# Kernel optimization log

Measured on AMD Instinct MI355X. Metric: run time of the kernel, lower is better.

The kernel has to match this reference:

```python
import jax, jax.numpy as jnp
import numpy as np

MARGIN = 0.5
BETA, GAMMA = 0.5, 0.2   # hard-coded in _get_triplet_selection_function
NUM_ANCHORS = 30          # hard-coded in select()
EPS_COS = 1e-8

B, C, D = 320, 80, 128


def setup_inputs() -> dict:
    key = jax.random.key(0)
    k1, k2, k3 = jax.random.split(key, 3)
    label = jax.random.randint(k1, (B, C), 0, 2).astype(jnp.int32)
    source = jax.random.normal(k2, (B, D), dtype=jnp.float32)
    target = jax.random.normal(k3, (B, D), dtype=jnp.float32)
    return {"label": label, "source": source, "target": target}


def _cos_distance(src, tgt):
    # F.cosine_similarity(src.unsqueeze(1), tgt, dim=-1): [B, B] sim matrix
    ns = jnp.linalg.norm(src, axis=-1)          # [B]
    nt = jnp.linalg.norm(tgt, axis=-1)          # [B]
    sim = (src @ tgt.T) / jnp.maximum(ns[:, None] * nt[None, :], EPS_COS)
    return jnp.clip(1.0 - sim, 0.0)


def _label_distances(labels_f):
    dot = labels_f @ labels_f.T                 # [B, B]
    sn = jnp.sqrt(jnp.diagonal(dot))            # [B]
    norms = sn[None, :] * sn[:, None]
    return 1.0 - jnp.minimum(1.0, dot / norms)


def _base_mask(b):
    ine = ~jnp.eye(b, dtype=bool)               # indices_not_equal
    # (a!=p) & (a!=n) & (p!=n)  ->  [B, B, B]
    return ine[:, :, None] & ine[:, None, :] & ine[None, :, :]


def _anchor_mask(fd, num_anchors):
    # select_diverse_anchors: pick the num_anchors anchors with the largest
    # mean feature distance to all other samples (most "diverse").
    diversity = jnp.mean(fd, axis=1)            # [B]
    _, idx = jax.lax.top_k(diversity, num_anchors)
    m = jnp.zeros((fd.shape[0],), dtype=bool).at[idx].set(True)
    return m[:, None, None]                     # broadcastable over (a, p, n)


def _triplet_mask(ld, beta, gamma):
    # select_triplets_smartly: (a, p) must be label-similar (dist <= gamma)
    # and (a, n) must be label-dissimilar (dist >= beta).
    pos = ld <= gamma                           # [B, B] over (a, p)
    neg = ld >= beta                            # [B, B] over (a, n)
    return pos[:, :, None] & neg[:, None, :]


def reference(label, source, target):
    fd = _cos_distance(source, target)                       # [B, B]
    ld = _label_distances(label.astype(jnp.float32))         # [B, B]
    mask = (_base_mask(fd.shape[0])
            & _anchor_mask(fd, NUM_ANCHORS)
            & _triplet_mask(ld, BETA, GAMMA))                # [B, B, B]
    # triplet_loss[a,p,n] = fd[a,p] - fd[a,n] + margin
    tl = fd[:, :, None] - fd[:, None, :] + MARGIN
    tl = jnp.clip(jnp.where(mask, tl, 0.0), 0.0)
    num_pos = jnp.sum(mask.astype(jnp.float32))
    return jnp.sum(tl) / (num_pos + 1e-4)
```

## Files before the change

kernel.cpp:

```cpp
#include <hip/hip_runtime.h>
#include <cstdint>

namespace {

constexpr int NB = 320;
constexpr int ND = 128;
constexpr int NC = 80;
constexpr int NANCH = 30;
constexpr int NW = 5;

constexpr size_t OFF_DIV  = 0;
constexpr size_t OFF_ASUM = 1280;
constexpr size_t OFF_ACNT = 3840;
constexpr size_t OFF_PACK = 5120;
constexpr size_t OFF_TGTT = 10240;

__global__ __launch_bounds__(256) void k_prep(
    const float* __restrict__ tgt,
    const int* __restrict__ label,
    float4* __restrict__ tgtT4,
    unsigned long long* __restrict__ packed)
{
    const int tid = threadIdx.x;
    const int w = tid >> 6, lane = tid & 63;
    const int r0 = blockIdx.x * 8;

    __shared__ float4 tile4[8][33];

    {
        const int r = r0 + w;
        int l0 = label[r * NC + lane];
        int l1 = (lane < NC - 64) ? label[r * NC + 64 + lane] : 0;
        unsigned long long b0 = __ballot(l0 != 0);
        unsigned long long b1 = __ballot(l1 != 0);
        if (lane == 0) { packed[2 * r] = b0; packed[2 * r + 1] = b1; }

        const int r2 = r0 + 4 + w;
        l0 = label[r2 * NC + lane];
        l1 = (lane < NC - 64) ? label[r2 * NC + 64 + lane] : 0;
        b0 = __ballot(l0 != 0);
        b1 = __ballot(l1 != 0);
        if (lane == 0) { packed[2 * r2] = b0; packed[2 * r2 + 1] = b1; }
    }

    {
        const int r = tid >> 5, d4 = tid & 31;
        tile4[r][d4] = reinterpret_cast<const float4*>(tgt)[(r0 + r) * 32 + d4];
    }
    __syncthreads();
    {
        const int rr = tid & 7, d4 = tid >> 3;
        tgtT4[d4 * NB + r0 + rr] = tile4[rr][d4];
    }
}

__global__ __launch_bounds__(256) void k_main(
    const float* __restrict__ src,
    const float4* __restrict__ tgtT4,
    const unsigned long long* __restrict__ packed,
    float* __restrict__ divr,
    double* __restrict__ asum,
    int* __restrict__ acnt)
{
    const int a = blockIdx.x;
    const int tid = threadIdx.x;
    const int w = tid >> 6, lane = tid & 63;

    __shared__ float sa[ND];
    __shared__ float snsa;
    __shared__ float red[256];
    __shared__ unsigned long long pk[2 * NB];
    __shared__ float fdrow[NB];
    __shared__ unsigned long long pmask[NW], nmask[NW];
    __shared__ double wsum[4];

    if (tid < ND) sa[tid] = src[a * ND + tid];
    if (w == 0) {
        float s0 = src[a * ND + lane];
        float s1 = src[a * ND + lane + 64];
        float v = s0 * s0 + s1 * s1;
        for (int off = 32; off > 0; off >>= 1) v += __shfl_down(v, off);
        if (lane == 0) snsa = sqrtf(v);
    }
    for (int q = tid; q < 2 * NB; q += 256) pk[q] = packed[q];
    __syncthreads();

    const unsigned long long a0 = pk[2 * a], a1 = pk[2 * a + 1];
    const float nsa = snsa;

    float acc = 0.f;
#pragma unroll
    for (int it = 0; it < 2; ++it) {
        const int j = tid + 256 * it;
        if (j < NB) {
            float dot = 0.f, tn = 0.f;
#pragma unroll
            for (int d = 0; d < ND / 4; ++d) {
                float4 t = tgtT4[d * NB + j];
                dot += sa[4 * d + 0] * t.x + sa[4 * d + 1] * t.y +
                       sa[4 * d + 2] * t.z + sa[4 * d + 3] * t.w;
                tn += t.x * t.x + t.y * t.y + t.z * t.z + t.w * t.w;
            }
            float sim = dot / fmaxf(nsa * sqrtf(tn), 1e-8f);
            float f = fmaxf(1.0f - sim, 0.0f);
            fdrow[j] = f;
            acc += f;
        }
    }

    red[tid] = acc;
    __syncthreads();
    for (int st = 128; st > 0; st >>= 1) {
        if (tid < st) red[tid] += red[tid + st];
        __syncthreads();
    }
    if (tid == 0) divr[a] = red[0] / (float)NB;

    const float sna = sqrtf((float)(__popcll(a0) + __popcll(a1)));
#pragma unroll
    for (int it = 0; it < 2; ++it) {
        const int jj = tid + 256 * it;
        if (jj < NB) {
            const unsigned long long j0 = pk[2 * jj], j1 = pk[2 * jj + 1];
            const float snj = sqrtf((float)(__popcll(j0) + __popcll(j1)));
            const float denom = sna * snj;
            const float dotf = (float)(__popcll(a0 & j0) + __popcll(a1 & j1));
            const float ld = 1.0f - fminf(1.0f, dotf / denom);
            const bool valid = (jj != a) && (denom > 0.f);
            unsigned long long pb = __ballot(valid && (ld <= 0.2f));
            unsigned long long nb = __ballot(valid && (ld >= 0.5f));
            if (lane == 0) { pmask[jj >> 6] = pb; nmask[jj >> 6] = nb; }
        }
    }
    __syncthreads();

    double s = 0.0;
#pragma unroll
    for (int it = 0; it < 2; ++it) {
        const int jj = tid + 256 * it;
        if (jj < NB && ((nmask[jj >> 6] >> (jj & 63)) & 1ull)) {
            const float fn = fdrow[jj];
#pragma unroll
            for (int wd = 0; wd < NW; ++wd) {
                unsigned long long m = pmask[wd];
                while (m) {
                    const int b = __builtin_ctzll(m);
                    m &= m - 1;
                    float v = fdrow[wd * 64 + b] - fn + 0.5f;
                    if (v > 0.f) s += (double)v;
                }
            }
        }
    }
    for (int off = 32; off > 0; off >>= 1) s += __shfl_down(s, off);
    if (lane == 0) wsum[w] = s;
    __syncthreads();
    if (tid == 0) {
        int P = 0, N = 0;
#pragma unroll
        for (int wd = 0; wd < NW; ++wd) {
            P += __popcll(pmask[wd]);
            N += __popcll(nmask[wd]);
        }
        asum[a] = wsum[0] + wsum[1] + wsum[2] + wsum[3];
        acnt[a] = P * N;
    }
}

__global__ __launch_bounds__(320) void k_final(
    const float* __restrict__ divr,
    const double* __restrict__ asum,
    const int* __restrict__ acnt,
    float* __restrict__ out)
{
    const int tid = threadIdx.x;
    __shared__ float dv[NB];
    __shared__ int alist[NANCH];
    __shared__ double sl[NANCH];
    __shared__ int cl[NANCH];

    dv[tid] = divr[tid];
    __syncthreads();

    const float ve = dv[tid];
    int rank = 0;
#pragma unroll 8
    for (int j = 0; j < NB; ++j) {
        float vj = dv[j];
        rank += (vj > ve) || (vj == ve && j < tid);
    }
    if (rank < NANCH) alist[rank] = tid;
    __syncthreads();

    if (tid < NANCH) {
        sl[tid] = asum[alist[tid]];
        cl[tid] = acnt[alist[tid]];
    }
    __syncthreads();
    if (tid == 0) {
        double S = 0.0;
        long long C = 0;
        for (int r = 0; r < NANCH; ++r) { S += sl[r]; C += cl[r]; }
        out[0] = (float)(S / ((double)C + 1e-4));
    }
}

}

extern "C" void kernel_launch(void* const* d_in, const int* in_sizes, int n_in,
                              void* d_out, int out_size, void* d_ws, size_t ws_size,
                              hipStream_t stream) {
    const int* label = (const int*)d_in[0];
    const float* src = (const float*)d_in[1];
    const float* tgt = (const float*)d_in[2];

    char* ws = (char*)d_ws;
    float* divr  = (float*)(ws + OFF_DIV);
    double* asum = (double*)(ws + OFF_ASUM);
    int* acnt    = (int*)(ws + OFF_ACNT);
    unsigned long long* packed = (unsigned long long*)(ws + OFF_PACK);
    float4* tgtT4 = (float4*)(ws + OFF_TGTT);

    k_prep <<<40, 256, 0, stream>>>(tgt, label, tgtT4, packed);
    k_main <<<NB, 256, 0, stream>>>(src, tgtT4, packed, divr, asum, acnt);
    k_final<<<1, 320, 0, stream>>>(divr, asum, acnt, (float*)d_out);
}
```

Baseline: 29.67 us.

## Fuse final top-k reduction into main kernel via last-block atomic counter

Removes the separate k_final launch by having each k_main block increment a global counter after writing its results. The last block to finish then performs the anchor ranking and final reduction. It also drops staging of the packed label bitmasks in shared memory, reading them straight from global memory instead. This saves one kernel launch and its gap, at the cost of a serial tail inside the last block plus extra fences and atomics.

```diff
diff --git a/kernel.cpp b/kernel.cpp
--- a/kernel.cpp
+++ b/kernel.cpp
@@ -14,18 +14,22 @@
 constexpr size_t OFF_ACNT = 3840;
 constexpr size_t OFF_PACK = 5120;
 constexpr size_t OFF_TGTT = 10240;
+constexpr size_t OFF_CTR  = 174080;
 
 __global__ __launch_bounds__(256) void k_prep(
     const float* __restrict__ tgt,
     const int* __restrict__ label,
     float4* __restrict__ tgtT4,
-    unsigned long long* __restrict__ packed)
+    unsigned long long* __restrict__ packed,
+    unsigned int* __restrict__ ctr)
 {
     const int tid = threadIdx.x;
     const int w = tid >> 6, lane = tid & 63;
     const int r0 = blockIdx.x * 8;
 
     __shared__ float4 tile4[8][33];
+
+    if (blockIdx.x == 0 && tid == 0) *ctr = 0;
 
     {
         const int r = r0 + w;
@@ -60,7 +64,9 @@
     const unsigned long long* __restrict__ packed,
     float* __restrict__ divr,
     double* __restrict__ asum,
-    int* __restrict__ acnt)
+    int* __restrict__ acnt,
+    unsigned int* __restrict__ ctr,
+    float* __restrict__ out)
 {
     const int a = blockIdx.x;
     const int tid = threadIdx.x;
@@ -69,10 +75,14 @@
     __shared__ float sa[ND];
     __shared__ float snsa;
     __shared__ float red[256];
-    __shared__ unsigned long long pk[2 * NB];
     __shared__ float fdrow[NB];
     __shared__ unsigned long long pmask[NW], nmask[NW];
     __shared__ double wsum[4];
+    __shared__ int isLastS;
+    __shared__ float dv[NB];
+    __shared__ int alist[NANCH];
+    __shared__ double sl[NANCH];
+    __shared__ int cl[NANCH];
 
     if (tid < ND) sa[tid] = src[a * ND + tid];
     if (w == 0) {
@@ -82,10 +92,8 @@
         for (int off = 32; off > 0; off >>= 1) v += __shfl_down(v, off);
         if (lane == 0) snsa = sqrtf(v);
     }
-    for (int q = tid; q < 2 * NB; q += 256) pk[q] = packed[q];
-    __syncthreads();
-
-    const unsigned long long a0 = pk[2 * a], a1 = pk[2 * a + 1];
+    __syncthreads();
+
     const float nsa = snsa;
 
     float acc = 0.f;
@@ -116,12 +124,13 @@
     }
     if (tid == 0) divr[a] = red[0] / (float)NB;
 
+    const unsigned long long a0 = packed[2 * a], a1 = packed[2 * a + 1];
     const float sna = sqrtf((float)(__popcll(a0) + __popcll(a1)));
 #pragma unroll
     for (int it = 0; it < 2; ++it) {
         const int jj = tid + 256 * it;
         if (jj < NB) {
-            const unsigned long long j0 = pk[2 * jj], j1 = pk[2 * jj + 1];
+            const unsigned long long j0 = packed[2 * jj], j1 = packed[2 * jj + 1];
             const float snj = sqrtf((float)(__popcll(j0) + __popcll(j1)));
             const float denom = sna * snj;
             const float dotf = (float)(__popcll(a0 & j0) + __popcll(a1 & j1));
@@ -164,34 +173,30 @@
         }
         asum[a] = wsum[0] + wsum[1] + wsum[2] + wsum[3];
         acnt[a] = P * N;
-    }
-}
-
-__global__ __launch_bounds__(320) void k_final(
-    const float* __restrict__ divr,
-    const double* __restrict__ asum,
-    const int* __restrict__ acnt,
-    float* __restrict__ out)
-{
-    const int tid = threadIdx.x;
-    __shared__ float dv[NB];
-    __shared__ int alist[NANCH];
-    __shared__ double sl[NANCH];
-    __shared__ int cl[NANCH];
-
-    dv[tid] = divr[tid];
-    __syncthreads();
-
-    const float ve = dv[tid];
-    int rank = 0;
+        __threadfence();
+        isLastS = (atomicAdd(ctr, 1u) == (unsigned)(NB - 1));
+    }
+    __syncthreads();
+    if (!isLastS) return;
+    __threadfence();
+
+    for (int q = tid; q < NB; q += 256) dv[q] = divr[q];
+    __syncthreads();
+#pragma unroll
+    for (int it = 0; it < 2; ++it) {
+        const int e = tid + 256 * it;
+        if (e < NB) {
+            const float ve = dv[e];
+            int rank = 0;
 #pragma unroll 8
-    for (int j = 0; j < NB; ++j) {
-        float vj = dv[j];
-        rank += (vj > ve) || (vj == ve && j < tid);
-    }
-    if (rank < NANCH) alist[rank] = tid;
-    __syncthreads();
-
+            for (int j = 0; j < NB; ++j) {
+                float vj = dv[j];
+                rank += (vj > ve) || (vj == ve && j < e);
+            }
+            if (rank < NANCH) alist[rank] = e;
+        }
+    }
+    __syncthreads();
     if (tid < NANCH) {
         sl[tid] = asum[alist[tid]];
         cl[tid] = acnt[alist[tid]];
@@ -220,8 +225,9 @@
     int* acnt    = (int*)(ws + OFF_ACNT);
     unsigned long long* packed = (unsigned long long*)(ws + OFF_PACK);
     float4* tgtT4 = (float4*)(ws + OFF_TGTT);
-
-    k_prep <<<40, 256, 0, stream>>>(tgt, label, tgtT4, packed);
-    k_main <<<NB, 256, 0, stream>>>(src, tgtT4, packed, divr, asum, acnt);
-    k_final<<<1, 320, 0, stream>>>(divr, asum, acnt, (float*)d_out);
-}
+    unsigned int* ctr = (unsigned int*)(ws + OFF_CTR);
+
+    k_prep<<<40, 256, 0, stream>>>(tgt, label, tgtT4, packed, ctr);
+    k_main<<<NB, 256, 0, stream>>>(src, tgtT4, packed, divr, asum, acnt, ctr,
+                                   (float*)d_out);
+}
```

New measurement: 40.07 us. +35.0%, slower.

## Map one thread per column in k_main with 320-thread blocks and wave reductions

Applied to the files above, without the earlier changes.

Launches k_main with 320 threads so each thread owns exactly one of the B columns, removing the two-iteration loops with their partial-wave tail. The shared-memory tree reduction for the diversity row sum becomes a wave shuffle reduction plus a five-entry combine. The bulk copy of packed labels into shared memory is replaced by direct global loads. Fewer barriers and less LDS traffic are the aim, at the cost of a fifth wave per block and uncached global reads of the packed labels.

```diff
diff --git a/kernel.cpp b/kernel.cpp
--- a/kernel.cpp
+++ b/kernel.cpp
@@ -54,7 +54,7 @@
     }
 }
 
-__global__ __launch_bounds__(256) void k_main(
+__global__ __launch_bounds__(320) void k_main(
     const float* __restrict__ src,
     const float4* __restrict__ tgtT4,
     const unsigned long long* __restrict__ packed,
@@ -68,11 +68,10 @@
 
     __shared__ float sa[ND];
     __shared__ float snsa;
-    __shared__ float red[256];
-    __shared__ unsigned long long pk[2 * NB];
     __shared__ float fdrow[NB];
     __shared__ unsigned long long pmask[NW], nmask[NW];
-    __shared__ double wsum[4];
+    __shared__ float wred[NW];
+    __shared__ double wsum[NW];
 
     if (tid < ND) sa[tid] = src[a * ND + tid];
     if (w == 0) {
@@ -82,64 +81,50 @@
         for (int off = 32; off > 0; off >>= 1) v += __shfl_down(v, off);
         if (lane == 0) snsa = sqrtf(v);
     }
-    for (int q = tid; q < 2 * NB; q += 256) pk[q] = packed[q];
-    __syncthreads();
-
-    const unsigned long long a0 = pk[2 * a], a1 = pk[2 * a + 1];
+    __syncthreads();
+
     const float nsa = snsa;
 
-    float acc = 0.f;
+    {
+        float dot = 0.f, tn = 0.f;
 #pragma unroll
-    for (int it = 0; it < 2; ++it) {
-        const int j = tid + 256 * it;
-        if (j < NB) {
-            float dot = 0.f, tn = 0.f;
-#pragma unroll
-            for (int d = 0; d < ND / 4; ++d) {
-                float4 t = tgtT4[d * NB + j];
-                dot += sa[4 * d + 0] * t.x + sa[4 * d + 1] * t.y +
-                       sa[4 * d + 2] * t.z + sa[4 * d + 3] * t.w;
-                tn += t.x * t.x + t.y * t.y + t.z * t.z + t.w * t.w;
-            }
-            float sim = dot / fmaxf(nsa * sqrtf(tn), 1e-8f);
-            float f = fmaxf(1.0f - sim, 0.0f);
-            fdrow[j] = f;
-            acc += f;
+        for (int d = 0; d < ND / 4; ++d) {
+            float4 t = tgtT4[d * NB + tid];
+            dot += sa[4 * d + 0] * t.x + sa[4 * d + 1] * t.y +
+                   sa[4 * d + 2] * t.z + sa[4 * d + 3] * t.w;
+            tn += t.x * t.x + t.y * t.y + t.z * t.z + t.w * t.w;
         }
-    }
-
-    red[tid] = acc;
-    __syncthreads();
-    for (int st = 128; st > 0; st >>= 1) {
-        if (tid < st) red[tid] += red[tid + st];
-        __syncthreads();
-    }
-    if (tid == 0) divr[a] = red[0] / (float)NB;
-
+        float sim = dot / fmaxf(nsa * sqrtf(tn), 1e-8f);
+        float f = fmaxf(1.0f - sim, 0.0f);
+        fdrow[tid] = f;
+        float af = f;
+        for (int off = 32; off > 0; off >>= 1) af += __shfl_down(af, off);
+        if (lane == 0) wred[w] = af;
+    }
+
+    const unsigned long long a0 = packed[2 * a], a1 = packed[2 * a + 1];
     const float sna = sqrtf((float)(__popcll(a0) + __popcll(a1)));
-#pragma unroll
-    for (int it = 0; it < 2; ++it) {
-        const int jj = tid + 256 * it;
-        if (jj < NB) {
-            const unsigned long long j0 = pk[2 * jj], j1 = pk[2 * jj + 1];
-            const float snj = sqrtf((float)(__popcll(j0) + __popcll(j1)));
-            const float denom = sna * snj;
-            const float dotf = (float)(__popcll(a0 & j0) + __popcll(a1 & j1));
-            const float ld = 1.0f - fminf(1.0f, dotf / denom);
-            const bool valid = (jj != a) && (denom > 0.f);
-            unsigned long long pb = __ballot(valid && (ld <= 0.2f));
-            unsigned long long nb = __ballot(valid && (ld >= 0.5f));
-            if (lane == 0) { pmask[jj >> 6] = pb; nmask[jj >> 6] = nb; }
-        }
-    }
-    __syncthreads();
-
-    double s = 0.0;
-#pragma unroll
-    for (int it = 0; it < 2; ++it) {
-        const int jj = tid + 256 * it;
-        if (jj < NB && ((nmask[jj >> 6] >> (jj & 63)) & 1ull)) {
-            const float fn = fdrow[jj];
+    {
+        const unsigned long long j0 = packed[2 * tid], j1 = packed[2 * tid + 1];
+        const float snj = sqrtf((float)(__popcll(j0) + __popcll(j1)));
+        const float denom = sna * snj;
+        const float dotf = (float)(__popcll(a0 & j0) + __popcll(a1 & j1));
+        const float ld = 1.0f - fminf(1.0f, dotf / denom);
+        const bool valid = (tid != a) && (denom > 0.f);
+        unsigned long long pb = __ballot(valid && (ld <= 0.2f));
+        unsigned long long nb = __ballot(valid && (ld >= 0.5f));
+        if (lane == 0) { pmask[w] = pb; nmask[w] = nb; }
+    }
+    __syncthreads();
+
+    if (tid == 0)
+        divr[a] = (wred[0] + wred[1] + wred[2] + wred[3] + wred[4]) / (float)NB;
+
+    {
+        double s = 0.0;
+        const bool nbit = (nmask[w] >> lane) & 1ull;
+        if (__ballot(nbit)) {
+            const float fn = fdrow[tid];
 #pragma unroll
             for (int wd = 0; wd < NW; ++wd) {
                 unsigned long long m = pmask[wd];
@@ -147,14 +132,15 @@
                     const int b = __builtin_ctzll(m);
                     m &= m - 1;
                     float v = fdrow[wd * 64 + b] - fn + 0.5f;
-                    if (v > 0.f) s += (double)v;
+                    if (nbit && v > 0.f) s += (double)v;
                 }
             }
         }
-    }
-    for (int off = 32; off > 0; off >>= 1) s += __shfl_down(s, off);
-    if (lane == 0) wsum[w] = s;
-    __syncthreads();
+        for (int off = 32; off > 0; off >>= 1) s += __shfl_down(s, off);
+        if (lane == 0) wsum[w] = s;
+    }
+    __syncthreads();
+
     if (tid == 0) {
         int P = 0, N = 0;
 #pragma unroll
@@ -162,7 +148,7 @@
             P += __popcll(pmask[wd]);
             N += __popcll(nmask[wd]);
         }
-        asum[a] = wsum[0] + wsum[1] + wsum[2] + wsum[3];
+        asum[a] = wsum[0] + wsum[1] + wsum[2] + wsum[3] + wsum[4];
         acnt[a] = P * N;
     }
 }
@@ -222,6 +208,6 @@
     float4* tgtT4 = (float4*)(ws + OFF_TGTT);
 
     k_prep <<<40, 256, 0, stream>>>(tgt, label, tgtT4, packed);
-    k_main <<<NB, 256, 0, stream>>>(src, tgtT4, packed, divr, asum, acnt);
+    k_main <<<NB, 320, 0, stream>>>(src, tgtT4, packed, divr, asum, acnt);
     k_final<<<1, 320, 0, stream>>>(divr, asum, acnt, (float*)d_out);
 }
```

Result: faster. 26.17 us, median of 2 (-11.8%).
